# Kernel optimization log

Hardware: AMD Instinct MI355X
Metric: run time of the kernel (lower is better)

Reference implementation:

```python
import jax, jax.numpy as jnp
import numpy as np


def setup_inputs() -> dict:
    key = jax.random.key(0)
    k1, k2 = jax.random.split(key)
    N, M, D = 16384, 16384, 3
    src_V = jax.random.normal(k1, (N, D), dtype=jnp.float32)
    tar_V = jax.random.normal(k2, (M, D), dtype=jnp.float32)
    return {"src_V": src_V, "tar_V": tar_V}


def reference(src_V, tar_V):
    # 1-NN: for each target point find nearest source point (replaces cKDTree).
    # Squared distances via ||t||^2 - 2 t.s + ||s||^2 ; [M, N]
    d2 = (
        jnp.sum(tar_V * tar_V, axis=1, keepdims=True)
        - 2.0 * (tar_V @ src_V.T)
        + jnp.sum(src_V * src_V, axis=1)[None, :]
    )
    ii = jnp.argmin(d2, axis=1)            # [M] nearest src index per target
    diff = src_V[ii] - tar_V               # [M, 3]
    loss = 0.5 * jnp.sum(diff * diff)
    return loss
```

## Files before the change

### kernel.cpp

```cpp
#include <hip/hip_runtime.h>
#include <math.h>

constexpr int N_SRC = 16384;
constexpr int M_TAR = 16384;

constexpr int BLOCKS = M_TAR / 32;
constexpr int TPB = 1024;
constexpr int CHUNKS = 256;
constexpr int TILE = 2048;
constexpr int TILES = N_SRC / TILE;
constexpr int ROWS_PT = TILE / CHUNKS;
constexpr int IPT = ROWS_PT / 2;

__global__ void zero_out(float* __restrict__ out) {
    if (threadIdx.x == 0) out[0] = 0.0f;
}

__device__ __forceinline__ float embed_ao(float t, unsigned mask_v, unsigned row_s) {
    float r;
    asm("v_and_or_b32 %0, %1, %2, %3"
        : "=v"(r) : "v"(t), "v"(mask_v), "s"(row_s));
    return r;
}
__device__ __forceinline__ void min3(float& b, float e0, float e1) {
    asm("v_min3_f32 %0, %0, %1, %2"
        : "+v"(b) : "v"(e0), "v"(e1));
}

__global__ __launch_bounds__(TPB, 8) void nn7(const float* __restrict__ src,
                                              const float* __restrict__ tar,
                                              float* __restrict__ out) {
    __shared__ float4 tile[2 * TILE];

    const int tid   = threadIdx.x;
    const int g     = tid & 3;
    const int chunk = tid >> 2;
    const int tbase = blockIdx.x * 32;

    float txm2[8], tym2[8], tzm2[8], best[8];
#pragma unroll
    for (int k = 0; k < 8; ++k) {
        int T = tbase + g + 4 * k;
        txm2[k] = -2.0f * tar[3 * T + 0];
        tym2[k] = -2.0f * tar[3 * T + 1];
        tzm2[k] = -2.0f * tar[3 * T + 2];
        best[k] = INFINITY;
    }

    {
        const float* q0 = src + 3 * tid;
        const float* q1 = src + 3 * (tid + TPB);
        float x0 = q0[0], y0 = q0[1], z0 = q0[2];
        float x1 = q1[0], y1 = q1[1], z1 = q1[2];
        tile[tid]       = make_float4(x0, y0, z0, fmaf(x0, x0, fmaf(y0, y0, z0 * z0)));
        tile[tid + TPB] = make_float4(x1, y1, z1, fmaf(x1, x1, fmaf(y1, y1, z1 * z1)));
    }
    __syncthreads();

    unsigned mask_v = 0xFFFFFFC0u;

#pragma unroll
    for (int tl = 0; tl < TILES; ++tl) {
        float x0, y0, z0, x1, y1, z1;
        if (tl + 1 < TILES) {
            const float* q0 = src + 3 * ((tl + 1) * TILE + tid);
            const float* q1 = q0 + 3 * TPB;
            x0 = q0[0]; y0 = q0[1]; z0 = q0[2];
            x1 = q1[0]; y1 = q1[1]; z1 = q1[2];
            __builtin_amdgcn_sched_barrier(0);
        }

        const int cb = (tl & 1) * TILE;
#pragma unroll
        for (int i = 0; i < IPT; ++i) {
            float4 s0 = tile[cb + (2 * i + 0) * CHUNKS + chunk];
            float4 s1 = tile[cb + (2 * i + 1) * CHUNKS + chunk];
            unsigned row0 = (unsigned)(tl * ROWS_PT + 2 * i + 0);
            unsigned row1 = row0 + 1;
#pragma unroll
            for (int k = 0; k < 8; ++k) {
                float t0 = fmaf(s0.z, tzm2[k], s0.w);
                t0 = fmaf(s0.y, tym2[k], t0);
                t0 = fmaf(s0.x, txm2[k], t0);
                float t1 = fmaf(s1.z, tzm2[k], s1.w);
                t1 = fmaf(s1.y, tym2[k], t1);
                t1 = fmaf(s1.x, txm2[k], t1);
                float e0 = embed_ao(t0, mask_v, row0);
                float e1 = embed_ao(t1, mask_v, row1);
                min3(best[k], e0, e1);
            }
        }

        if (tl + 1 < TILES) {
            const int wb = ((tl + 1) & 1) * TILE;
            tile[wb + tid]       = make_float4(x0, y0, z0, fmaf(x0, x0, fmaf(y0, y0, z0 * z0)));
            tile[wb + tid + TPB] = make_float4(x1, y1, z1, fmaf(x1, x1, fmaf(y1, y1, z1 * z1)));
        }
        __syncthreads();
    }

    float* fv = (float*)tile;
    int*   fj = (int*)tile + 32 * 256;
#pragma unroll
    for (int k = 0; k < 8; ++k) {
        unsigned b = __float_as_uint(best[k]);
        int j  = (int)((b & 63u) * CHUNKS + chunk);
        int lt = g + 4 * k;
        fv[lt * CHUNKS + chunk] = __uint_as_float(b & 0xFFFFFFC0u);
        fj[lt * CHUNKS + chunk] = j;
    }
    __syncthreads();

    const int tprime = tid >> 5;
    const int sub    = tid & 31;
    float bv = fv[tprime * CHUNKS + sub];
    int   bj = fj[tprime * CHUNKS + sub];
#pragma unroll
    for (int m = 1; m < 8; ++m) {
        float v = fv[tprime * CHUNKS + sub + 32 * m];
        int   j = fj[tprime * CHUNKS + sub + 32 * m];
        if (v < bv) { bv = v; bj = j; }
    }
#pragma unroll
    for (int s = 16; s >= 1; s >>= 1) {
        float vv = __shfl_xor(bv, s, 64);
        int   jj = __shfl_xor(bj, s, 64);
        if (vv < bv) { bv = vv; bj = jj; }
    }
    __syncthreads();

    if (sub == 0) {
        int tt = tbase + tprime;
        float dx = src[3 * bj + 0] - tar[3 * tt + 0];
        float dy = src[3 * bj + 1] - tar[3 * tt + 1];
        float dz = src[3 * bj + 2] - tar[3 * tt + 2];
        fv[tprime] = 0.5f * fmaf(dx, dx, fmaf(dy, dy, dz * dz));
    }
    __syncthreads();
    if (tid == 0) {
        float ssum = 0.0f;
#pragma unroll
        for (int i = 0; i < 32; ++i) ssum += fv[i];
        atomicAdd(out, ssum);
    }
}

extern "C" void kernel_launch(void* const* d_in, const int* in_sizes, int n_in,
                              void* d_out, int out_size, void* d_ws, size_t ws_size,
                              hipStream_t stream) {
    const float* src = (const float*)d_in[0];
    const float* tar = (const float*)d_in[1];
    float* out = (float*)d_out;
    (void)d_ws; (void)ws_size;

    zero_out<<<1, 64, 0, stream>>>(out);
    nn7<<<BLOCKS, TPB, 0, stream>>>(src, tar, out);
}
```

Baseline: 86.05 us.

## Halve block size and give each thread sixteen targets instead of eight

Blocks drop from 1024 to 512 threads and each thread now tracks 16 contiguous targets, so each shared-memory source load is reused across twice as many targets. Each thread therefore stages four source points per tile instead of two. The tile loop is no longer unrolled, the last tile is handled outside the loop, and the final reduction is adjusted for 16 lanes per target. The cost is more registers per thread and fewer threads available to hide latency, and the occupancy hint in launch bounds drops from 8 to 4.

```diff
diff --git a/kernel.cpp b/kernel.cpp
--- a/kernel.cpp
+++ b/kernel.cpp
@@ -4,13 +4,15 @@
 constexpr int N_SRC = 16384;
 constexpr int M_TAR = 16384;
 
-constexpr int BLOCKS = M_TAR / 32;
-constexpr int TPB = 1024;
+constexpr int BLOCKS = 512;
+constexpr int TPB = 512;
 constexpr int CHUNKS = 256;
 constexpr int TILE = 2048;
 constexpr int TILES = N_SRC / TILE;
 constexpr int ROWS_PT = TILE / CHUNKS;
 constexpr int IPT = ROWS_PT / 2;
+constexpr int TPT = 16;
+constexpr int PPT = TILE / TPB;
 
 __global__ void zero_out(float* __restrict__ out) {
     if (threadIdx.x == 0) out[0] = 0.0f;
@@ -27,58 +29,46 @@
         : "+v"(b) : "v"(e0), "v"(e1));
 }
 
-__global__ __launch_bounds__(TPB, 8) void nn7(const float* __restrict__ src,
+__global__ __launch_bounds__(TPB, 4) void nn8(const float* __restrict__ src,
                                               const float* __restrict__ tar,
                                               float* __restrict__ out) {
     __shared__ float4 tile[2 * TILE];
 
     const int tid   = threadIdx.x;
-    const int g     = tid & 3;
-    const int chunk = tid >> 2;
+    const int g     = tid >> 8;
+    const int chunk = tid & 255;
     const int tbase = blockIdx.x * 32;
 
-    float txm2[8], tym2[8], tzm2[8], best[8];
+    float txm2[TPT], tym2[TPT], tzm2[TPT], best[TPT];
 #pragma unroll
-    for (int k = 0; k < 8; ++k) {
-        int T = tbase + g + 4 * k;
+    for (int k = 0; k < TPT; ++k) {
+        int T = tbase + g * TPT + k;
         txm2[k] = -2.0f * tar[3 * T + 0];
         tym2[k] = -2.0f * tar[3 * T + 1];
         tzm2[k] = -2.0f * tar[3 * T + 2];
         best[k] = INFINITY;
     }
 
-    {
-        const float* q0 = src + 3 * tid;
-        const float* q1 = src + 3 * (tid + TPB);
-        float x0 = q0[0], y0 = q0[1], z0 = q0[2];
-        float x1 = q1[0], y1 = q1[1], z1 = q1[2];
-        tile[tid]       = make_float4(x0, y0, z0, fmaf(x0, x0, fmaf(y0, y0, z0 * z0)));
-        tile[tid + TPB] = make_float4(x1, y1, z1, fmaf(x1, x1, fmaf(y1, y1, z1 * z1)));
+#pragma unroll
+    for (int r = 0; r < PPT; ++r) {
+        int p = tid + r * TPB;
+        const float* q = src + 3 * p;
+        float x = q[0], y = q[1], z = q[2];
+        tile[p] = make_float4(x, y, z, fmaf(x, x, fmaf(y, y, z * z)));
     }
     __syncthreads();
 
     unsigned mask_v = 0xFFFFFFC0u;
 
-#pragma unroll
-    for (int tl = 0; tl < TILES; ++tl) {
-        float x0, y0, z0, x1, y1, z1;
-        if (tl + 1 < TILES) {
-            const float* q0 = src + 3 * ((tl + 1) * TILE + tid);
-            const float* q1 = q0 + 3 * TPB;
-            x0 = q0[0]; y0 = q0[1]; z0 = q0[2];
-            x1 = q1[0]; y1 = q1[1]; z1 = q1[2];
-            __builtin_amdgcn_sched_barrier(0);
-        }
-
-        const int cb = (tl & 1) * TILE;
+    auto compute = [&](int cb, unsigned rowbase) {
 #pragma unroll
         for (int i = 0; i < IPT; ++i) {
             float4 s0 = tile[cb + (2 * i + 0) * CHUNKS + chunk];
             float4 s1 = tile[cb + (2 * i + 1) * CHUNKS + chunk];
-            unsigned row0 = (unsigned)(tl * ROWS_PT + 2 * i + 0);
-            unsigned row1 = row0 + 1;
+            unsigned row0 = rowbase + 2 * i;
+            unsigned row1 = rowbase + 2 * i + 1;
 #pragma unroll
-            for (int k = 0; k < 8; ++k) {
+            for (int k = 0; k < TPT; ++k) {
                 float t0 = fmaf(s0.z, tzm2[k], s0.w);
                 t0 = fmaf(s0.y, tym2[k], t0);
                 t0 = fmaf(s0.x, txm2[k], t0);
@@ -90,39 +80,56 @@
                 min3(best[k], e0, e1);
             }
         }
+    };
 
-        if (tl + 1 < TILES) {
-            const int wb = ((tl + 1) & 1) * TILE;
-            tile[wb + tid]       = make_float4(x0, y0, z0, fmaf(x0, x0, fmaf(y0, y0, z0 * z0)));
-            tile[wb + tid + TPB] = make_float4(x1, y1, z1, fmaf(x1, x1, fmaf(y1, y1, z1 * z1)));
+#pragma unroll 1
+    for (int tl = 0; tl < TILES - 1; ++tl) {
+        float px[PPT], py[PPT], pz[PPT];
+#pragma unroll
+        for (int r = 0; r < PPT; ++r) {
+            const float* q = src + 3 * ((tl + 1) * TILE + tid + r * TPB);
+            px[r] = q[0]; py[r] = q[1]; pz[r] = q[2];
+        }
+        __builtin_amdgcn_sched_barrier(0);
+
+        compute((tl & 1) * TILE, (unsigned)(tl * ROWS_PT));
+
+        const int wb = ((tl + 1) & 1) * TILE;
+#pragma unroll
+        for (int r = 0; r < PPT; ++r) {
+            float x = px[r], y = py[r], z = pz[r];
+            tile[wb + tid + r * TPB] =
+                make_float4(x, y, z, fmaf(x, x, fmaf(y, y, z * z)));
         }
         __syncthreads();
     }
+    compute(((TILES - 1) & 1) * TILE, (unsigned)((TILES - 1) * ROWS_PT));
 
+    __syncthreads();
     float* fv = (float*)tile;
     int*   fj = (int*)tile + 32 * 256;
 #pragma unroll
-    for (int k = 0; k < 8; ++k) {
+    for (int k = 0; k < TPT; ++k) {
         unsigned b = __float_as_uint(best[k]);
         int j  = (int)((b & 63u) * CHUNKS + chunk);
-        int lt = g + 4 * k;
+        int lt = g * TPT + k;
         fv[lt * CHUNKS + chunk] = __uint_as_float(b & 0xFFFFFFC0u);
         fj[lt * CHUNKS + chunk] = j;
     }
     __syncthreads();
 
-    const int tprime = tid >> 5;
-    const int sub    = tid & 31;
+    const int tprime = tid >> 4;
+    const int sub    = tid & 15;
     float bv = fv[tprime * CHUNKS + sub];
     int   bj = fj[tprime * CHUNKS + sub];
 #pragma unroll
-    for (int m = 1; m < 8; ++m) {
-        float v = fv[tprime * CHUNKS + sub + 32 * m];
-        int   j = fj[tprime * CHUNKS + sub + 32 * m];
+    for (int m = 1; m < CHUNKS / 16; ++m) {
+        float v = fv[tprime * CHUNKS + sub + 16 * m];
+        int   j = fj[tprime * CHUNKS + sub + 16 * m];
         if (v < bv) { bv = v; bj = j; }
     }
 #pragma unroll
-    for (int s = 16; s >= 1; s >>= 1) {
+    for (int s = 8; s >= 1; s >>= 1) {
         float vv = __shfl_xor(bv, s, 64);
         int   jj = __shfl_xor(bj, s, 64);
         if (vv < bv) { bv = vv; bj = jj; }
@@ -154,5 +161,5 @@
     (void)d_ws; (void)ws_size;
 
     zero_out<<<1, 64, 0, stream>>>(out);
-    nn7<<<BLOCKS, TPB, 0, stream>>>(src, tar, out);
+    nn8<<<BLOCKS, TPB, 0, stream>>>(src, tar, out);
 }
```

Result: no change. 87.68 us (+1.9%).
